# Performance work log

Measured on AMD Instinct MI355X. Metric: run time of the kernel, lower is better.

Reference implementation:

```python
import jax, jax.numpy as jnp
import numpy as np

EPS = 1e-5
BLEND = 0.5  # with prior_batchsize=0, x_iclm == x_bn so CNM == BatchNorm1d (training mode)


def batchnorm(x, gamma, beta):
    # torch BatchNorm1d training mode: batch mean, biased variance
    mean = x.mean(axis=0)
    var = x.var(axis=0)  # ddof=0 (biased), matching torch normalization
    xn = (x - mean) * jax.lax.rsqrt(var + EPS)
    return xn * gamma + beta


def ensemble_linear(x, W):
    # x: [B, D*F], W: [D, O, F] block-diagonal weights
    B = x.shape[0]
    D, O, F = W.shape
    xb = x.reshape(B, D, F)
    out = jnp.einsum('bdf,dof->bdo', xb, W)
    return out.reshape(B, D * O)


def setup_inputs() -> dict:
    key = jax.random.key(0)
    ks = jax.random.split(key, 3)
    B, F, D, O2 = 16384, 1024, 4, 32
    x = jax.random.normal(ks[0], (B, F), dtype=jnp.float32)
    # torch init: normal_(mean=0, std=0.0001) on linear weights
    W1 = jax.random.normal(ks[1], (D, F, F), dtype=jnp.float32) * 1e-4
    W2 = jax.random.normal(ks[2], (D, O2, F), dtype=jnp.float32) * 1e-4
    g1 = jnp.ones((D * F,), jnp.float32); b1 = jnp.zeros((D * F,), jnp.float32)
    g2 = jnp.ones((D * F,), jnp.float32); b2 = jnp.zeros((D * F,), jnp.float32)
    g3 = jnp.ones((D * O2,), jnp.float32); b3 = jnp.zeros((D * O2,), jnp.float32)
    return {"x": x, "W1": W1, "W2": W2, "g1": g1, "b1": b1,
            "g2": g2, "b2": b2, "g3": g3, "b3": b3}


def reference(x, W1, W2, g1, b1, g2, b2, g3, b3):
    D = W1.shape[0]
    h = jnp.concatenate([x] * D, axis=-1)          # [B, D*F]
    h = batchnorm(h, g1, b1)                        # CNM 1
    h = ensemble_linear(h, W1)                      # EnsembleLinear F->F
    h = jax.nn.sigmoid(batchnorm(h, g2, b2))        # CNM 2 + Sigmoid
    h = ensemble_linear(h, W2)                      # EnsembleLinear F->32
    h = jax.nn.sigmoid(batchnorm(h, g3, b3))        # CNM 3 + Sigmoid
    return h  # [B, D*32]
```

## Files before the change

kernel.cpp:

```cpp
#include <hip/hip_runtime.h>
#include <hip/hip_bf16.h>
#include <stdint.h>

#define B_N 16384
#define F_N 1024
#define D_N 4
#define O_N 32
#define NCOL1 (D_N * F_N)
#define NCOL2 (D_N * O_N)

static constexpr float EPS = 1e-5f;

typedef __bf16 bf16x8 __attribute__((ext_vector_type(8)));
typedef __bf16 bf16x4 __attribute__((ext_vector_type(4)));
typedef float  f32x4  __attribute__((ext_vector_type(4)));

#define GLD16(gp, lp)                                                          \
  __builtin_amdgcn_global_load_lds(                                            \
      (__attribute__((address_space(1))) void*)(uintptr_t)(gp),                \
      (__attribute__((address_space(3))) void*)(lp), 16, 0, 0)

__global__ __launch_bounds__(256) void k_stats_x_conv(
    const float* __restrict__ x, float* __restrict__ part,
    __bf16* __restrict__ xb) {
  int t = threadIdx.x, blk = blockIdx.x;
  const float4* xr = (const float4*)x;
  float s0 = 0, s1 = 0, s2 = 0, s3 = 0, q0 = 0, q1 = 0, q2 = 0, q3 = 0;
  int r0 = blk * 64;
  for (int r = r0; r < r0 + 64; ++r) {
    float4 v = xr[(size_t)r * (F_N / 4) + t];
    s0 += v.x; q0 += v.x * v.x;
    s1 += v.y; q1 += v.y * v.y;
    s2 += v.z; q2 += v.z * v.z;
    s3 += v.w; q3 += v.w * v.w;
    bf16x4 o;
    o[0] = (__bf16)v.x; o[1] = (__bf16)v.y; o[2] = (__bf16)v.z; o[3] = (__bf16)v.w;
    *(bf16x4*)(xb + (size_t)r * F_N + t * 4) = o;
  }
  float* p = part + (size_t)blk * 2048;
  p[t * 4 + 0] = s0; p[t * 4 + 1] = s1; p[t * 4 + 2] = s2; p[t * 4 + 3] = s3;
  p[1024 + t * 4 + 0] = q0; p[1024 + t * 4 + 1] = q1;
  p[1024 + t * 4 + 2] = q2; p[1024 + t * 4 + 3] = q3;
}

__global__ __launch_bounds__(256) void k_stats_x_final(
    const float* __restrict__ part, float* __restrict__ rstdx) {
  int c = blockIdx.x * 256 + threadIdx.x;
  float s = 0, q = 0;
  for (int b = 0; b < 256; ++b) {
    s += part[(size_t)b * 2048 + c];
    q += part[(size_t)b * 2048 + 1024 + c];
  }
  float mean = s * (1.0f / B_N);
  float var = q * (1.0f / B_N) - mean * mean;
  rstdx[c] = rsqrtf(var + EPS);
}

__global__ __launch_bounds__(256) void k_fold_w1(const float* __restrict__ W1,
                                                 const float* __restrict__ g1,
                                                 const float* __restrict__ rstdx,
                                                 __bf16* __restrict__ W1b) {
  size_t base = (size_t)(blockIdx.x * 256 + threadIdx.x) * 4;
  int f = (int)(base & (F_N - 1));
  int d = (int)(base >> 20);
  float4 w = *(const float4*)(W1 + base);
  float4 g = *(const float4*)(g1 + d * F_N + f);
  float4 r = *(const float4*)(rstdx + f);
  bf16x4 o;
  o[0] = (__bf16)(w.x * g.x * r.x); o[1] = (__bf16)(w.y * g.y * r.y);
  o[2] = (__bf16)(w.z * g.z * r.z); o[3] = (__bf16)(w.w * g.w * r.w);
  *(bf16x4*)(W1b + base) = o;
}

__global__ __launch_bounds__(256) void k_fold_w2(const float* __restrict__ W2,
                                                 __bf16* __restrict__ W2b) {
  size_t base = (size_t)(blockIdx.x * 256 + threadIdx.x) * 4;
  float4 w = *(const float4*)(W2 + base);
  bf16x4 o;
  o[0] = (__bf16)w.x; o[1] = (__bf16)w.y; o[2] = (__bf16)w.z; o[3] = (__bf16)w.w;
  *(bf16x4*)(W2b + base) = o;
}

__global__ __launch_bounds__(512, 2) void k_gemm1(
    const __bf16* __restrict__ A, const __bf16* __restrict__ Bw,
    __bf16* __restrict__ C, float* __restrict__ p2s, float* __restrict__ p2q) {
  __shared__ __bf16 ldsA[2][2][256 * 32];
  __shared__ __bf16 ldsB[2][2][256 * 32];
  const int tid = threadIdx.x;
  const int wave = tid >> 6, lane = tid & 63;
  const int wm = wave >> 2, wn = wave & 3;
  int bid = (int)blockIdx.x;
  const int c_ = bid & 7, q_ = bid >> 3;
  const int bm = c_ * 8 + (q_ >> 4), bn = q_ & 15;
  const int m0 = bm * 256, n0 = bn * 256;
  const int fr = lane & 15, kg = lane >> 4;
  const int swz8 = (kg ^ ((fr >> 1) & 3)) * 8;
  const int srow = tid >> 2;
  const int scb = ((tid & 3) ^ ((tid >> 3) & 3)) * 16;
  const char* Ab = (const char*)A + (size_t)(m0 + srow) * (F_N * 2) + scb;
  const char* Bb = (const char*)Bw + (size_t)(n0 + srow) * (F_N * 2) + scb;
  char* ldsAx = (char*)&ldsA[0][0][0];
  char* ldsBx = (char*)&ldsB[0][0][0];
  const int wo = wave * 1024;

#define SA(buf_, kk_, kb_)                                                     \
  do {                                                                         \
    GLD16(Ab + (kb_) + (kk_) * 64,                                             \
          ldsAx + (buf_) * 32768 + (kk_) * 16384 + wo);                        \
    GLD16(Ab + 128 * (F_N * 2) + (kb_) + (kk_) * 64,                           \
          ldsAx + (buf_) * 32768 + (kk_) * 16384 + 8192 + wo);                 \
  } while (0)
#define SBv(buf_, kk_, kb_)                                                    \
  do {                                                                         \
    GLD16(Bb + (kb_) + (kk_) * 64,                                             \
          ldsBx + (buf_) * 32768 + (kk_) * 16384 + wo);                        \
    GLD16(Bb + 128 * (F_N * 2) + (kb_) + (kk_) * 64,                           \
          ldsBx + (buf_) * 32768 + (kk_) * 16384 + 8192 + wo);                 \
  } while (0)
#define LDA4(dst_, buf_, kk_, qm_)                                             \
  { _Pragma("unroll") for (int i_ = 0; i_ < 4; ++i_)                           \
      dst_[i_] = *(const bf16x8*)&ldsA[buf_][kk_]                              \
          [(wm * 128 + (qm_) * 64 + i_ * 16 + fr) * 32 + swz8]; }
#define LDB4(dst_, buf_, kk_)                                                  \
  { _Pragma("unroll") for (int i_ = 0; i_ < 4; ++i_)                           \
      dst_[i_] = *(const bf16x8*)&ldsB[buf_][kk_]                              \
          [(wn * 64 + i_ * 16 + fr) * 32 + swz8]; }
#define MFMA16(a_, b_, qm_)                                                    \
  { _Pragma("unroll") for (int i_ = 0; i_ < 4; ++i_)                           \
      _Pragma("unroll") for (int j_ = 0; j_ < 4; ++j_)                         \
        acc[(qm_) * 4 + i_][j_] = __builtin_amdgcn_mfma_f32_16x16x32_bf16(     \
            a_[i_], b_[j_], acc[(qm_) * 4 + i_][j_], 0, 0, 0); }
#define BAR() __builtin_amdgcn_s_barrier()
#define SB0() __builtin_amdgcn_sched_barrier(0)
#define WAITVM4() asm volatile("s_waitcnt vmcnt(4)" ::: "memory")
#define PRIO1() __builtin_amdgcn_s_setprio(1)
#define PRIO0() __builtin_amdgcn_s_setprio(0)

  f32x4 acc[8][4] = {};
  bf16x8 afrE[4], afrO[4], bfrE[4], bfrO[4];

  SBv(0, 0, 0); SA(0, 0, 0); SBv(0, 1, 0); SA(0, 1, 0);
  asm volatile("s_waitcnt vmcnt(4)" ::: "memory");
  BAR(); SB0();
  LDA4(afrE, 0, 0, 0); LDB4(bfrE, 0, 0);

#define TILE(b_, nb_, kn_)                                                     \
  SBv(nb_, 0, kn_); BAR(); SB0();                                              \
  LDA4(afrO, b_, 0, 1);                                                        \
  PRIO1(); MFMA16(afrE, bfrE, 0); PRIO0();                                     \
  SA(nb_, 0, kn_); WAITVM4(); BAR(); SB0();                                    \
  LDA4(afrE, b_, 1, 0); LDB4(bfrO, b_, 1);                                     \
  PRIO1(); MFMA16(afrO, bfrE, 1); PRIO0();                                     \
  SBv(nb_, 1, kn_); BAR(); SB0();                                              \
  LDA4(afrO, b_, 1, 1);                                                        \
  PRIO1(); MFMA16(afrE, bfrO, 0); PRIO0();                                     \
  SA(nb_, 1, kn_); WAITVM4(); BAR(); SB0();                                    \
  LDA4(afrE, nb_, 0, 0); LDB4(bfrE, nb_, 0);                                   \
  PRIO1(); MFMA16(afrO, bfrO, 1); PRIO0();

  for (int t = 0; t < 16; t += 2) {
    const int kn1 = (t + 1) * 128;
    const int kn2 = (t + 2 < 16) ? (t + 2) * 128 : 0;
    TILE(0, 1, kn1)
    TILE(1, 0, kn2)
  }

  const int cr = kg * 4, cc = fr;
#pragma unroll
  for (int mi = 0; mi < 8; ++mi)
#pragma unroll
    for (int ni = 0; ni < 4; ++ni) {
      int row = m0 + wm * 128 + mi * 16 + cr;
      int col = n0 + wn * 64 + ni * 16 + cc;
#pragma unroll
      for (int r = 0; r < 4; ++r)
        C[(size_t)(row + r) * NCOL1 + col] = (__bf16)acc[mi][ni][r];
    }

  float* srs = (float*)&ldsA[1][0][0];
  float* srq = srs + 512;
  __syncthreads();
#pragma unroll
  for (int ni = 0; ni < 4; ++ni) {
    float ss = 0, qq = 0;
#pragma unroll
    for (int mi = 0; mi < 8; ++mi) {
      f32x4 v = acc[mi][ni];
#pragma unroll
      for (int r = 0; r < 4; ++r) { ss += v[r]; qq += v[r] * v[r]; }
    }
    ss += __shfl_xor(ss, 16); ss += __shfl_xor(ss, 32);
    qq += __shfl_xor(qq, 16); qq += __shfl_xor(qq, 32);
    if (lane < 16) {
      srs[wave * 64 + ni * 16 + lane] = ss;
      srq[wave * 64 + ni * 16 + lane] = qq;
    }
  }
  __syncthreads();
  if (tid < 256) {
    int j = tid, wnn = j >> 6, jj = j & 63;
    float S = srs[wnn * 64 + jj] + srs[(4 + wnn) * 64 + jj];
    float Q = srq[wnn * 64 + jj] + srq[(4 + wnn) * 64 + jj];
    p2s[(size_t)bm * NCOL1 + n0 + j] = S;
    p2q[(size_t)bm * NCOL1 + n0 + j] = Q;
  }
#undef SA
#undef SBv
#undef LDA4
#undef LDB4
#undef MFMA16
#undef TILE
#undef BAR
#undef SB0
#undef WAITVM4
#undef PRIO1
#undef PRIO0
}

__global__ __launch_bounds__(256) void k_stats2_final(
    const float* __restrict__ p2s, const float* __restrict__ p2q,
    const float* __restrict__ g2, const float* __restrict__ b2,
    float* __restrict__ a2, float* __restrict__ c2) {
  int c = blockIdx.x * 256 + threadIdx.x;
  float s = 0, q = 0;
  for (int b = 0; b < 64; ++b) {
    s += p2s[(size_t)b * NCOL1 + c];
    q += p2q[(size_t)b * NCOL1 + c];
  }
  float mean = s * (1.0f / B_N);
  float var = q * (1.0f / B_N) - mean * mean;
  float rstd = rsqrtf(var + EPS);
  float aa = rstd * g2[c];
  a2[c] = aa;
  c2[c] = b2[c] - mean * aa;
}

__global__ __launch_bounds__(256) void k_gemm2(
    const __bf16* __restrict__ G1, const __bf16* __restrict__ W2b,
    const float* __restrict__ a2, const float* __restrict__ c2,
    float* __restrict__ out2) {
  const int tid = threadIdx.x;
  const int wave = tid >> 6, lane = tid & 63;
  const int m0 = blockIdx.x * 64;
  const int d = blockIdx.y;
  const int fr = lane & 15, fk = (lane >> 4) * 8;
  const __bf16* Arow = G1 + (size_t)(m0 + wave * 16 + fr) * NCOL1 + d * F_N;
  const __bf16* Wd = W2b + (size_t)d * O_N * F_N;
  const float* ap = a2 + d * F_N;
  const float* cp = c2 + d * F_N;
  f32x4 acc[2] = {};
  for (int k0 = 0; k0 < F_N; k0 += 32) {
    bf16x8 av = *(const bf16x8*)(Arow + k0 + fk);
    f32x4 aa0 = *(const f32x4*)(ap + k0 + fk);
    f32x4 aa1 = *(const f32x4*)(ap + k0 + fk + 4);
    f32x4 cc0 = *(const f32x4*)(cp + k0 + fk);
    f32x4 cc1 = *(const f32x4*)(cp + k0 + fk + 4);
    bf16x8 af;
#pragma unroll
    for (int j = 0; j < 4; ++j) {
      float v = (float)av[j] * aa0[j] + cc0[j];
      af[j] = (__bf16)(1.0f / (1.0f + __expf(-v)));
    }
#pragma unroll
    for (int j = 0; j < 4; ++j) {
      float v = (float)av[4 + j] * aa1[j] + cc1[j];
      af[4 + j] = (__bf16)(1.0f / (1.0f + __expf(-v)));
    }
    bf16x8 b0 = *(const bf16x8*)(Wd + (size_t)fr * F_N + k0 + fk);
    bf16x8 b1 = *(const bf16x8*)(Wd + (size_t)(16 + fr) * F_N + k0 + fk);
    acc[0] = __builtin_amdgcn_mfma_f32_16x16x32_bf16(af, b0, acc[0], 0, 0, 0);
    acc[1] = __builtin_amdgcn_mfma_f32_16x16x32_bf16(af, b1, acc[1], 0, 0, 0);
  }
  const int cr = (lane >> 4) * 4, cc = lane & 15;
#pragma unroll
  for (int n = 0; n < 2; ++n)
#pragma unroll
    for (int r = 0; r < 4; ++r)
      out2[(size_t)(m0 + wave * 16 + cr + r) * NCOL2 + d * O_N + n * 16 + cc] =
          acc[n][r];
}

__global__ __launch_bounds__(128) void k_stats3_partial(
    const float* __restrict__ out2, float* __restrict__ part) {
  int t = threadIdx.x, blk = blockIdx.x;
  float s = 0, q = 0;
  int r0 = blk * 128;
  for (int r = r0; r < r0 + 128; ++r) {
    float v = out2[(size_t)r * NCOL2 + t];
    s += v;
    q += v * v;
  }
  part[(size_t)blk * 256 + t] = s;
  part[(size_t)blk * 256 + 128 + t] = q;
}

__global__ __launch_bounds__(128) void k_stats3_final(
    const float* __restrict__ part, const float* __restrict__ g3,
    const float* __restrict__ b3, float* __restrict__ a3,
    float* __restrict__ c3) {
  int c = threadIdx.x;
  float s = 0, q = 0;
  for (int b = 0; b < 128; ++b) {
    s += part[(size_t)b * 256 + c];
    q += part[(size_t)b * 256 + 128 + c];
  }
  float mean = s * (1.0f / B_N);
  float var = q * (1.0f / B_N) - mean * mean;
  float rstd = rsqrtf(var + EPS);
  float aa = rstd * g3[c];
  a3[c] = aa;
  c3[c] = b3[c] - mean * aa;
}

__global__ __launch_bounds__(256) void k_final(const float* __restrict__ out2,
                                               const float* __restrict__ a3,
                                               const float* __restrict__ c3,
                                               float* __restrict__ out) {
  size_t base = (size_t)(blockIdx.x * 256 + threadIdx.x) * 4;
  int c = (int)(base & (NCOL2 - 1));
  f32x4 v = *(const f32x4*)(out2 + base);
  f32x4 a = *(const f32x4*)(a3 + c);
  f32x4 cc = *(const f32x4*)(c3 + c);
  f32x4 o;
#pragma unroll
  for (int j = 0; j < 4; ++j)
    o[j] = 1.0f / (1.0f + __expf(-(v[j] * a[j] + cc[j])));
  *(f32x4*)(out + base) = o;
}

extern "C" void kernel_launch(void* const* d_in, const int* in_sizes, int n_in,
                              void* d_out, int out_size, void* d_ws,
                              size_t ws_size, hipStream_t stream) {
  (void)in_sizes; (void)n_in; (void)out_size; (void)ws_size;
  const float* x = (const float*)d_in[0];
  const float* W1 = (const float*)d_in[1];
  const float* W2 = (const float*)d_in[2];
  const float* g1 = (const float*)d_in[3];
  const float* g2 = (const float*)d_in[5];
  const float* b2 = (const float*)d_in[6];
  const float* g3 = (const float*)d_in[7];
  const float* b3 = (const float*)d_in[8];
  float* out = (float*)d_out;

  char* ws = (char*)d_ws;
  size_t off = 0;
  auto alloc = [&](size_t bytes) -> void* {
    void* p = ws + off;
    off = (off + bytes + 255) & ~(size_t)255;
    return p;
  };
  float* rstdx = (float*)alloc((size_t)F_N * 4);
  float* a2 = (float*)alloc((size_t)NCOL1 * 4);
  float* c2 = (float*)alloc((size_t)NCOL1 * 4);
  float* a3 = (float*)alloc((size_t)NCOL2 * 4);
  float* c3 = (float*)alloc((size_t)NCOL2 * 4);
  float* part1 = (float*)alloc((size_t)256 * 2048 * 4);
  float* p2s = (float*)alloc((size_t)64 * NCOL1 * 4);
  float* p2q = (float*)alloc((size_t)64 * NCOL1 * 4);
  float* part3 = (float*)alloc((size_t)128 * 256 * 4);
  __bf16* W1b = (__bf16*)alloc((size_t)D_N * F_N * F_N * 2);
  __bf16* W2b = (__bf16*)alloc((size_t)D_N * O_N * F_N * 2);
  __bf16* xb = (__bf16*)alloc((size_t)B_N * F_N * 2);
  __bf16* G1 = (__bf16*)alloc((size_t)B_N * NCOL1 * 2);
  float* out2 = (float*)alloc((size_t)B_N * NCOL2 * 4);

  k_stats_x_conv<<<256, 256, 0, stream>>>(x, part1, xb);
  k_stats_x_final<<<4, 256, 0, stream>>>(part1, rstdx);
  k_fold_w1<<<4096, 256, 0, stream>>>(W1, g1, rstdx, W1b);
  k_fold_w2<<<128, 256, 0, stream>>>(W2, W2b);
  k_gemm1<<<1024, 512, 0, stream>>>(xb, W1b, G1, p2s, p2q);
  k_stats2_final<<<16, 256, 0, stream>>>(p2s, p2q, g2, b2, a2, c2);
  k_gemm2<<<dim3(256, 4), 256, 0, stream>>>(G1, W2b, a2, c2, out2);
  k_stats3_partial<<<128, 128, 0, stream>>>(out2, part3);
  k_stats3_final<<<1, 128, 0, stream>>>(part3, g3, b3, a3, c3);
  k_final<<<2048, 256, 0, stream>>>(out2, a3, c3, out);
}
```

Before: 267.3 us.

## Restructure GEMM1 LDS pipeline into a 4-slot ring with deeper prefetch

Replaces the double-buffered (2 buffers × 2 k-halves) LDS staging in k_gemm1 with a 4-slot ring of 32-wide K chunks. Three chunks are prefetched up front and loads run two to three slots ahead, with vmcnt waits raised to 8 so more global-to-LDS loads stay in flight while MFMAs execute. An explicit epilogue drains the pipeline. It also unrolls the gemm2 K loop by 2; the deeper ring raises the risk of wrong wait counts or slot hazards.

```diff
diff --git a/kernel.cpp b/kernel.cpp
--- a/kernel.cpp
+++ b/kernel.cpp
@@ -84,8 +84,8 @@
 __global__ __launch_bounds__(512, 2) void k_gemm1(
     const __bf16* __restrict__ A, const __bf16* __restrict__ Bw,
     __bf16* __restrict__ C, float* __restrict__ p2s, float* __restrict__ p2q) {
-  __shared__ __bf16 ldsA[2][2][256 * 32];
-  __shared__ __bf16 ldsB[2][2][256 * 32];
+  __shared__ __bf16 ldsA[4][256 * 32];
+  __shared__ __bf16 ldsB[4][256 * 32];
   const int tid = threadIdx.x;
   const int wave = tid >> 6, lane = tid & 63;
   const int wm = wave >> 2, wn = wave & 3;
@@ -99,31 +99,27 @@
   const int scb = ((tid & 3) ^ ((tid >> 3) & 3)) * 16;
   const char* Ab = (const char*)A + (size_t)(m0 + srow) * (F_N * 2) + scb;
   const char* Bb = (const char*)Bw + (size_t)(n0 + srow) * (F_N * 2) + scb;
-  char* ldsAx = (char*)&ldsA[0][0][0];
-  char* ldsBx = (char*)&ldsB[0][0][0];
+  char* ldsAx = (char*)&ldsA[0][0];
+  char* ldsBx = (char*)&ldsB[0][0];
   const int wo = wave * 1024;
 
-#define SA(buf_, kk_, kb_)                                                     \
+#define SA(slot_, kb_)                                                         \
   do {                                                                         \
-    GLD16(Ab + (kb_) + (kk_) * 64,                                             \
-          ldsAx + (buf_) * 32768 + (kk_) * 16384 + wo);                        \
-    GLD16(Ab + 128 * (F_N * 2) + (kb_) + (kk_) * 64,                           \
-          ldsAx + (buf_) * 32768 + (kk_) * 16384 + 8192 + wo);                 \
+    GLD16(Ab + (kb_), ldsAx + (slot_) * 16384 + wo);                           \
+    GLD16(Ab + 128 * (F_N * 2) + (kb_), ldsAx + (slot_) * 16384 + 8192 + wo);  \
   } while (0)
-#define SBv(buf_, kk_, kb_)                                                    \
+#define SBv(slot_, kb_)                                                        \
   do {                                                                         \
-    GLD16(Bb + (kb_) + (kk_) * 64,                                             \
-          ldsBx + (buf_) * 32768 + (kk_) * 16384 + wo);                        \
-    GLD16(Bb + 128 * (F_N * 2) + (kb_) + (kk_) * 64,                           \
-          ldsBx + (buf_) * 32768 + (kk_) * 16384 + 8192 + wo);                 \
+    GLD16(Bb + (kb_), ldsBx + (slot_) * 16384 + wo);                           \
+    GLD16(Bb + 128 * (F_N * 2) + (kb_), ldsBx + (slot_) * 16384 + 8192 + wo);  \
   } while (0)
-#define LDA4(dst_, buf_, kk_, qm_)                                             \
+#define LDA4(dst_, slot_, qm_)                                                 \
   { _Pragma("unroll") for (int i_ = 0; i_ < 4; ++i_)                           \
-      dst_[i_] = *(const bf16x8*)&ldsA[buf_][kk_]                              \
+      dst_[i_] = *(const bf16x8*)&ldsA[slot_]                                  \
           [(wm * 128 + (qm_) * 64 + i_ * 16 + fr) * 32 + swz8]; }
-#define LDB4(dst_, buf_, kk_)                                                  \
+#define LDB4(dst_, slot_)                                                      \
   { _Pragma("unroll") for (int i_ = 0; i_ < 4; ++i_)                           \
-      dst_[i_] = *(const bf16x8*)&ldsB[buf_][kk_]                              \
+      dst_[i_] = *(const bf16x8*)&ldsB[slot_]                                  \
           [(wn * 64 + i_ * 16 + fr) * 32 + swz8]; }
 #define MFMA16(a_, b_, qm_)                                                    \
   { _Pragma("unroll") for (int i_ = 0; i_ < 4; ++i_)                           \
@@ -132,38 +128,45 @@
             a_[i_], b_[j_], acc[(qm_) * 4 + i_][j_], 0, 0, 0); }
 #define BAR() __builtin_amdgcn_s_barrier()
 #define SB0() __builtin_amdgcn_sched_barrier(0)
-#define WAITVM4() asm volatile("s_waitcnt vmcnt(4)" ::: "memory")
+#define WAITVM(n_) asm volatile("s_waitcnt vmcnt(" #n_ ")" ::: "memory")
 #define PRIO1() __builtin_amdgcn_s_setprio(1)
 #define PRIO0() __builtin_amdgcn_s_setprio(0)
 
   f32x4 acc[8][4] = {};
-  bf16x8 afrE[4], afrO[4], bfrE[4], bfrO[4];
-
-  SBv(0, 0, 0); SA(0, 0, 0); SBv(0, 1, 0); SA(0, 1, 0);
-  asm volatile("s_waitcnt vmcnt(4)" ::: "memory");
+  bf16x8 afr0[4], afr1[4], bfrE[4], bfrO[4];
+
+  SBv(0, 0);   SA(0, 0);
+  SBv(1, 64);  SA(1, 64);
+  SBv(2, 128); SA(2, 128);
+  WAITVM(8);
   BAR(); SB0();
-  LDA4(afrE, 0, 0, 0); LDB4(bfrE, 0, 0);
-
-#define TILE(b_, nb_, kn_)                                                     \
-  SBv(nb_, 0, kn_); BAR(); SB0();                                              \
-  LDA4(afrO, b_, 0, 1);                                                        \
-  PRIO1(); MFMA16(afrE, bfrE, 0); PRIO0();                                     \
-  SA(nb_, 0, kn_); WAITVM4(); BAR(); SB0();                                    \
-  LDA4(afrE, b_, 1, 0); LDB4(bfrO, b_, 1);                                     \
-  PRIO1(); MFMA16(afrO, bfrE, 1); PRIO0();                                     \
-  SBv(nb_, 1, kn_); BAR(); SB0();                                              \
-  LDA4(afrO, b_, 1, 1);                                                        \
-  PRIO1(); MFMA16(afrE, bfrO, 0); PRIO0();                                     \
-  SA(nb_, 1, kn_); WAITVM4(); BAR(); SB0();                                    \
-  LDA4(afrE, nb_, 0, 0); LDB4(bfrE, nb_, 0);                                   \
-  PRIO1(); MFMA16(afrO, bfrO, 1); PRIO0();
-
-  for (int t = 0; t < 16; t += 2) {
-    const int kn1 = (t + 1) * 128;
-    const int kn2 = (t + 2 < 16) ? (t + 2) * 128 : 0;
-    TILE(0, 1, kn1)
-    TILE(1, 0, kn2)
-  }
+  LDA4(afr0, 0, 0); LDB4(bfrE, 0);
+
+#define PH1(rb_, sb_, BC_, kb_, SOK_)                                          \
+  if (SOK_) { SBv(sb_, kb_); }                                                 \
+  BAR(); SB0();                                                                \
+  LDA4(afr1, rb_, 1);                                                          \
+  PRIO1(); MFMA16(afr0, BC_, 0); PRIO0();
+#define PH2(nrb_, sb_, BC_, BN_, kb_, SOK_, VN_)                               \
+  if (SOK_) { SA(sb_, kb_); }                                                  \
+  WAITVM(VN_);                                                                 \
+  BAR(); SB0();                                                                \
+  LDA4(afr0, nrb_, 0); LDB4(BN_, nrb_);                                        \
+  PRIO1(); MFMA16(afr1, BC_, 1); PRIO0();
+
+  for (int T = 0; T < 28; T += 4) {
+    const int kb0 = (T + 3) * 64, kb1 = (T + 4) * 64;
+    const int kb2 = (T + 5) * 64, kb3 = (T + 6) * 64;
+    PH1(0, 3, bfrE, kb0, 1) PH2(1, 3, bfrE, bfrO, kb0, 1, 8)
+    PH1(1, 0, bfrO, kb1, 1) PH2(2, 0, bfrO, bfrE, kb1, 1, 8)
+    PH1(2, 1, bfrE, kb2, 1) PH2(3, 1, bfrE, bfrO, kb2, 1, 8)
+    PH1(3, 2, bfrO, kb3, 1) PH2(0, 2, bfrO, bfrE, kb3, 1, 8)
+  }
+  PH1(0, 3, bfrE, 1984, 1) PH2(1, 3, bfrE, bfrO, 1984, 1, 8)
+  PH1(1, 0, bfrO, 0, 0)    PH2(2, 0, bfrO, bfrE, 0, 0, 4)
+  PH1(2, 1, bfrE, 0, 0)    PH2(3, 1, bfrE, bfrO, 0, 0, 0)
+  PH1(3, 2, bfrO, 0, 0)
+  PRIO1(); MFMA16(afr1, bfrO, 1); PRIO0();
 
   const int cr = kg * 4, cc = fr;
 #pragma unroll
@@ -177,7 +180,7 @@
         C[(size_t)(row + r) * NCOL1 + col] = (__bf16)acc[mi][ni][r];
     }
 
-  float* srs = (float*)&ldsA[1][0][0];
+  float* srs = (float*)&ldsA[0][0];
   float* srq = srs + 512;
   __syncthreads();
 #pragma unroll
@@ -209,10 +212,11 @@
 #undef LDA4
 #undef LDB4
 #undef MFMA16
-#undef TILE
+#undef PH1
+#undef PH2
 #undef BAR
 #undef SB0
-#undef WAITVM4
+#undef WAITVM
 #undef PRIO1
 #undef PRIO0
 }
@@ -249,6 +253,7 @@
   const float* ap = a2 + d * F_N;
   const float* cp = c2 + d * F_N;
   f32x4 acc[2] = {};
+#pragma unroll 2
   for (int k0 = 0; k0 < F_N; k0 += 32) {
     bf16x8 av = *(const bf16x8*)(Arow + k0 + fk);
     f32x4 aa0 = *(const f32x4*)(ap + k0 + fk);
```

Result: no change. 270.5 us (+1.2%).

## Fuse W2 conversion into prep kernel and layer-3 stats into gemm2 epilogue

Applied to the files above, without the earlier changes.

Merges the W2 bf16 conversion into the x stats/convert kernel as extra blocks, and doubles the x-stats grid to 512 blocks of 32 rows for more parallelism. Computes layer-3 column sums and sums of squares in the gemm2 epilogue using shuffles and LDS, which removes the separate stats3_partial pass over out2. Also unrolls the gemm2 K loop by two. The costs are a larger partial buffer for the x stats, a longer final reduction over 512 partials, and an extra __syncthreads in gemm2.

```diff
diff --git a/kernel.cpp b/kernel.cpp
--- a/kernel.cpp
+++ b/kernel.cpp
@@ -20,34 +20,43 @@
       (__attribute__((address_space(1))) void*)(uintptr_t)(gp),                \
       (__attribute__((address_space(3))) void*)(lp), 16, 0, 0)
 
-__global__ __launch_bounds__(256) void k_stats_x_conv(
+__global__ __launch_bounds__(256) void k_pre(
     const float* __restrict__ x, float* __restrict__ part,
-    __bf16* __restrict__ xb) {
+    __bf16* __restrict__ xb, const float* __restrict__ W2,
+    __bf16* __restrict__ W2b) {
   int t = threadIdx.x, blk = blockIdx.x;
-  const float4* xr = (const float4*)x;
-  float s0 = 0, s1 = 0, s2 = 0, s3 = 0, q0 = 0, q1 = 0, q2 = 0, q3 = 0;
-  int r0 = blk * 64;
-  for (int r = r0; r < r0 + 64; ++r) {
-    float4 v = xr[(size_t)r * (F_N / 4) + t];
-    s0 += v.x; q0 += v.x * v.x;
-    s1 += v.y; q1 += v.y * v.y;
-    s2 += v.z; q2 += v.z * v.z;
-    s3 += v.w; q3 += v.w * v.w;
+  if (blk < 512) {
+    const float4* xr = (const float4*)x;
+    float s0 = 0, s1 = 0, s2 = 0, s3 = 0, q0 = 0, q1 = 0, q2 = 0, q3 = 0;
+    int r0 = blk * 32;
+    for (int r = r0; r < r0 + 32; ++r) {
+      float4 v = xr[(size_t)r * (F_N / 4) + t];
+      s0 += v.x; q0 += v.x * v.x;
+      s1 += v.y; q1 += v.y * v.y;
+      s2 += v.z; q2 += v.z * v.z;
+      s3 += v.w; q3 += v.w * v.w;
+      bf16x4 o;
+      o[0] = (__bf16)v.x; o[1] = (__bf16)v.y; o[2] = (__bf16)v.z; o[3] = (__bf16)v.w;
+      *(bf16x4*)(xb + (size_t)r * F_N + t * 4) = o;
+    }
+    float* p = part + (size_t)blk * 2048;
+    p[t * 4 + 0] = s0; p[t * 4 + 1] = s1; p[t * 4 + 2] = s2; p[t * 4 + 3] = s3;
+    p[1024 + t * 4 + 0] = q0; p[1024 + t * 4 + 1] = q1;
+    p[1024 + t * 4 + 2] = q2; p[1024 + t * 4 + 3] = q3;
+  } else {
+    size_t base = (size_t)((blk - 512) * 256 + t) * 4;
+    float4 w = *(const float4*)(W2 + base);
     bf16x4 o;
-    o[0] = (__bf16)v.x; o[1] = (__bf16)v.y; o[2] = (__bf16)v.z; o[3] = (__bf16)v.w;
-    *(bf16x4*)(xb + (size_t)r * F_N + t * 4) = o;
-  }
-  float* p = part + (size_t)blk * 2048;
-  p[t * 4 + 0] = s0; p[t * 4 + 1] = s1; p[t * 4 + 2] = s2; p[t * 4 + 3] = s3;
-  p[1024 + t * 4 + 0] = q0; p[1024 + t * 4 + 1] = q1;
-  p[1024 + t * 4 + 2] = q2; p[1024 + t * 4 + 3] = q3;
+    o[0] = (__bf16)w.x; o[1] = (__bf16)w.y; o[2] = (__bf16)w.z; o[3] = (__bf16)w.w;
+    *(bf16x4*)(W2b + base) = o;
+  }
 }
 
 __global__ __launch_bounds__(256) void k_stats_x_final(
     const float* __restrict__ part, float* __restrict__ rstdx) {
   int c = blockIdx.x * 256 + threadIdx.x;
   float s = 0, q = 0;
-  for (int b = 0; b < 256; ++b) {
+  for (int b = 0; b < 512; ++b) {
     s += part[(size_t)b * 2048 + c];
     q += part[(size_t)b * 2048 + 1024 + c];
   }
@@ -70,15 +79,6 @@
   o[0] = (__bf16)(w.x * g.x * r.x); o[1] = (__bf16)(w.y * g.y * r.y);
   o[2] = (__bf16)(w.z * g.z * r.z); o[3] = (__bf16)(w.w * g.w * r.w);
   *(bf16x4*)(W1b + base) = o;
-}
-
-__global__ __launch_bounds__(256) void k_fold_w2(const float* __restrict__ W2,
-                                                 __bf16* __restrict__ W2b) {
-  size_t base = (size_t)(blockIdx.x * 256 + threadIdx.x) * 4;
-  float4 w = *(const float4*)(W2 + base);
-  bf16x4 o;
-  o[0] = (__bf16)w.x; o[1] = (__bf16)w.y; o[2] = (__bf16)w.z; o[3] = (__bf16)w.w;
-  *(bf16x4*)(W2b + base) = o;
 }
 
 __global__ __launch_bounds__(512, 2) void k_gemm1(
@@ -238,7 +238,9 @@
 __global__ __launch_bounds__(256) void k_gemm2(
     const __bf16* __restrict__ G1, const __bf16* __restrict__ W2b,
     const float* __restrict__ a2, const float* __restrict__ c2,
-    float* __restrict__ out2) {
+    float* __restrict__ out2, float* __restrict__ p3s,
+    float* __restrict__ p3q) {
+  __shared__ float sred[2][4][2][16];
   const int tid = threadIdx.x;
   const int wave = tid >> 6, lane = tid & 63;
   const int m0 = blockIdx.x * 64;
@@ -249,6 +251,7 @@
   const float* ap = a2 + d * F_N;
   const float* cp = c2 + d * F_N;
   f32x4 acc[2] = {};
+#pragma unroll 2
   for (int k0 = 0; k0 < F_N; k0 += 32) {
     bf16x8 av = *(const bf16x8*)(Arow + k0 + fk);
     f32x4 aa0 = *(const f32x4*)(ap + k0 + fk);
@@ -278,31 +281,41 @@
     for (int r = 0; r < 4; ++r)
       out2[(size_t)(m0 + wave * 16 + cr + r) * NCOL2 + d * O_N + n * 16 + cc] =
           acc[n][r];
-}
-
-__global__ __launch_bounds__(128) void k_stats3_partial(
-    const float* __restrict__ out2, float* __restrict__ part) {
-  int t = threadIdx.x, blk = blockIdx.x;
-  float s = 0, q = 0;
-  int r0 = blk * 128;
-  for (int r = r0; r < r0 + 128; ++r) {
-    float v = out2[(size_t)r * NCOL2 + t];
-    s += v;
-    q += v * v;
-  }
-  part[(size_t)blk * 256 + t] = s;
-  part[(size_t)blk * 256 + 128 + t] = q;
+
+#pragma unroll
+  for (int n = 0; n < 2; ++n) {
+    float s = acc[n][0] + acc[n][1] + acc[n][2] + acc[n][3];
+    float q = acc[n][0] * acc[n][0] + acc[n][1] * acc[n][1] +
+              acc[n][2] * acc[n][2] + acc[n][3] * acc[n][3];
+    s += __shfl_xor(s, 16); s += __shfl_xor(s, 32);
+    q += __shfl_xor(q, 16); q += __shfl_xor(q, 32);
+    if (lane < 16) {
+      sred[0][wave][n][lane] = s;
+      sred[1][wave][n][lane] = q;
+    }
+  }
+  __syncthreads();
+  if (tid < 32) {
+    int n = tid >> 4, c = tid & 15;
+    float S = sred[0][0][n][c] + sred[0][1][n][c] + sred[0][2][n][c] +
+              sred[0][3][n][c];
+    float Q = sred[1][0][n][c] + sred[1][1][n][c] + sred[1][2][n][c] +
+              sred[1][3][n][c];
+    int col = d * O_N + n * 16 + c;
+    p3s[(size_t)blockIdx.x * NCOL2 + col] = S;
+    p3q[(size_t)blockIdx.x * NCOL2 + col] = Q;
+  }
 }
 
 __global__ __launch_bounds__(128) void k_stats3_final(
-    const float* __restrict__ part, const float* __restrict__ g3,
-    const float* __restrict__ b3, float* __restrict__ a3,
-    float* __restrict__ c3) {
+    const float* __restrict__ p3s, const float* __restrict__ p3q,
+    const float* __restrict__ g3, const float* __restrict__ b3,
+    float* __restrict__ a3, float* __restrict__ c3) {
   int c = threadIdx.x;
   float s = 0, q = 0;
-  for (int b = 0; b < 128; ++b) {
-    s += part[(size_t)b * 256 + c];
-    q += part[(size_t)b * 256 + 128 + c];
+  for (int b = 0; b < 256; ++b) {
+    s += p3s[(size_t)b * NCOL2 + c];
+    q += p3q[(size_t)b * NCOL2 + c];
   }
   float mean = s * (1.0f / B_N);
   float var = q * (1.0f / B_N) - mean * mean;
@@ -354,24 +367,23 @@
   float* c2 = (float*)alloc((size_t)NCOL1 * 4);
   float* a3 = (float*)alloc((size_t)NCOL2 * 4);
   float* c3 = (float*)alloc((size_t)NCOL2 * 4);
-  float* part1 = (float*)alloc((size_t)256 * 2048 * 4);
+  float* part1 = (float*)alloc((size_t)512 * 2048 * 4);
   float* p2s = (float*)alloc((size_t)64 * NCOL1 * 4);
   float* p2q = (float*)alloc((size_t)64 * NCOL1 * 4);
-  float* part3 = (float*)alloc((size_t)128 * 256 * 4);
+  float* p3s = (float*)alloc((size_t)256 * NCOL2 * 4);
+  float* p3q = (float*)alloc((size_t)256 * NCOL2 * 4);
   __bf16* W1b = (__bf16*)alloc((size_t)D_N * F_N * F_N * 2);
   __bf16* W2b = (__bf16*)alloc((size_t)D_N * O_N * F_N * 2);
   __bf16* xb = (__bf16*)alloc((size_t)B_N * F_N * 2);
   __bf16* G1 = (__bf16*)alloc((size_t)B_N * NCOL1 * 2);
   float* out2 = (float*)alloc((size_t)B_N * NCOL2 * 4);
 
-  k_stats_x_conv<<<256, 256, 0, stream>>>(x, part1, xb);
+  k_pre<<<640, 256, 0, stream>>>(x, part1, xb, W2, W2b);
   k_stats_x_final<<<4, 256, 0, stream>>>(part1, rstdx);
   k_fold_w1<<<4096, 256, 0, stream>>>(W1, g1, rstdx, W1b);
-  k_fold_w2<<<128, 256, 0, stream>>>(W2, W2b);
   k_gemm1<<<1024, 512, 0, stream>>>(xb, W1b, G1, p2s, p2q);
   k_stats2_final<<<16, 256, 0, stream>>>(p2s, p2q, g2, b2, a2, c2);
-  k_gemm2<<<dim3(256, 4), 256, 0, stream>>>(G1, W2b, a2, c2, out2);
-  k_stats3_partial<<<128, 128, 0, stream>>>(out2, part3);
-  k_stats3_final<<<1, 128, 0, stream>>>(part3, g3, b3, a3, c3);
+  k_gemm2<<<dim3(256, 4), 256, 0, stream>>>(G1, W2b, a2, c2, out2, p3s, p3q);
+  k_stats3_final<<<1, 128, 0, stream>>>(p3s, p3q, g3, b3, a3, c3);
   k_final<<<2048, 256, 0, stream>>>(out2, a3, c3, out);
 }
```

Result: slower. 287.4 us (+7.5%).
